# Optimization experiments

Hardware: AMD Instinct MI355X
Metric: run time of the kernel (lower is better)

Reference implementation:

```python
import jax, jax.numpy as jnp
import numpy as np


def setup_inputs() -> dict:
    key = jax.random.key(0)
    k1, k2, k3, k4 = jax.random.split(key, 4)
    B, C_in, C_out, E, K = 4, 128, 256, 30000, 5
    x = jax.random.normal(k1, (B, C_in, E, 1), dtype=jnp.float32)
    ne_idx = jax.random.randint(k2, (B, E, K - 1), 0, E, dtype=jnp.int32)
    conv_w = jax.random.normal(k3, (C_out, C_in, 1, K), dtype=jnp.float32) * 0.05
    conv_b = jax.random.normal(k4, (C_out,), dtype=jnp.float32) * 0.05
    return {"x": x, "ne_idx": ne_idx, "conv_w": conv_w, "conv_b": conv_b}


def reference(x, ne_idx, conv_w, conv_b):
    # x: [B, C, E, 1] edge features; ne_idx: [B, E, 4] neighbor edge ids.
    B, C, E, _ = x.shape
    xs = x[..., 0]                                        # [B, C, E]

    # pad_graph_mat: prepend self index column -> [B, E, 5]
    self_idx = jnp.broadcast_to(
        jnp.arange(E, dtype=ne_idx.dtype)[None, :, None], (B, E, 1))
    idx = jnp.concatenate([self_idx, ne_idx], axis=2) + 1  # +1 for zero pad slot

    # zero-pad feature dim so index 0 maps to zeros (matches torch padding col)
    x_pad = jnp.pad(xs, ((0, 0), (0, 0), (1, 0)))          # [B, C, E+1]

    # gather: f[b, c, e, k] = x_pad[b, c, idx[b, e, k]]
    f = jax.vmap(lambda xp, i: xp[:, i])(x_pad, idx)       # [B, C, E, 5]

    e0, e1, e2, e3, e4 = (f[..., j] for j in range(5))
    p = e1 + e3
    q = e2 + e4
    p1 = jnp.abs(e1 - e3)
    q1 = jnp.abs(e2 - e4)
    G = jnp.stack([e0, p, q, p1, q1], axis=-1)             # [B, C, E, 5]

    # Conv2d with kernel (1, 5): contraction over in-channels and the 5 taps
    out = jnp.einsum('bcek,ocuk->boe', G, conv_w) + conv_b[None, :, None]
    return out[..., None]                                  # [B, C_out, E, 1]
```

## Files before the change

kernel.cpp:

```cpp
#include <hip/hip_runtime.h>
#include <hip/hip_bf16.h>
#include <stdint.h>

#define E_N   30000
#define C_IN  128
#define C_OUT 256
#define B_N   4
#define KTAP  5
#define BN    64

typedef short bf16x8 __attribute__((ext_vector_type(8)));
typedef float f32x4  __attribute__((ext_vector_type(4)));

static __device__ __forceinline__ unsigned short f2bf(float f) {
    union { float f; uint32_t u; } v; v.f = f;
    uint32_t r = (v.u + 0x7FFFu + ((v.u >> 16) & 1u)) >> 16;
    return (unsigned short)r;
}
static __device__ __forceinline__ float bf2f(uint32_t h) {
    union { uint32_t u; float f; } v; v.u = h << 16;
    return v.f;
}

static __device__ __forceinline__ void comb8(const uint4& u, const uint4& v,
                                             uint4& s, uint4& d) {
    const uint32_t* a = (const uint32_t*)&u;
    const uint32_t* b = (const uint32_t*)&v;
    uint32_t* so = (uint32_t*)&s;
    uint32_t* dr = (uint32_t*)&d;
#pragma unroll
    for (int i = 0; i < 4; ++i) {
        float x0 = bf2f(a[i] & 0xFFFFu), x1 = bf2f(a[i] >> 16);
        float y0 = bf2f(b[i] & 0xFFFFu), y1 = bf2f(b[i] >> 16);
        so[i] = (uint32_t)f2bf(x0 + y0) | ((uint32_t)f2bf(x1 + y1) << 16);
        dr[i] = (uint32_t)f2bf(fabsf(x0 - y0)) | ((uint32_t)f2bf(fabsf(x1 - y1)) << 16);
    }
}

__global__ void pack_w_kernel(const float* __restrict__ w,
                              unsigned short* __restrict__ wp) {
    int tid = blockIdx.x * blockDim.x + threadIdx.x;
    if (tid >= 20 * 16 * 64) return;
    int s    = tid >> 10;
    int mt   = (tid >> 6) & 15;
    int lane = tid & 63;
    int m    = mt * 16 + (lane & 15);
    int kb   = s * 32 + ((lane >> 4) & 3) * 8;
    uint32_t pv[4];
    for (int jj = 0; jj < 4; ++jj) {
        unsigned short lo, hi;
        {
            int kk = kb + 2 * jj;
            int t = kk >> 7, c = kk & 127;
            lo = f2bf(w[(m * C_IN + c) * KTAP + t]);
        }
        {
            int kk = kb + 2 * jj + 1;
            int t = kk >> 7, c = kk & 127;
            hi = f2bf(w[(m * C_IN + c) * KTAP + t]);
        }
        pv[jj] = (uint32_t)lo | ((uint32_t)hi << 16);
    }
    uint4 val; val.x = pv[0]; val.y = pv[1]; val.z = pv[2]; val.w = pv[3];
    *(uint4*)(wp + (size_t)tid * 8) = val;
}

__global__ void transpose_kernel(const float* __restrict__ x,
                                 unsigned short* __restrict__ xT) {
    __shared__ float ld[C_IN][64 + 1];
    int b  = blockIdx.y;
    int e0 = blockIdx.x * 64;
    int t  = threadIdx.x;
    bool full = (e0 + 64 <= E_N);
    for (int pass = 0; pass < 8; ++pass) {
        int c  = pass * 16 + (t >> 4);
        int eo = (t & 15) * 4;
        if (full) {
            const float4 v = *(const float4*)(x + ((size_t)(b * C_IN + c) * E_N + e0 + eo));
            ld[c][eo] = v.x; ld[c][eo + 1] = v.y; ld[c][eo + 2] = v.z; ld[c][eo + 3] = v.w;
        } else {
            for (int i = 0; i < 4; ++i) {
                int e = e0 + eo + i;
                ld[c][eo + i] = (e < E_N) ? x[(size_t)(b * C_IN + c) * E_N + e] : 0.f;
            }
        }
    }
    __syncthreads();
    for (int pass = 0; pass < 4; ++pass) {
        int el = pass * 16 + (t >> 4);
        int c0 = (t & 15) * 8;
        int e  = e0 + el;
        if (e < E_N) {
            uint32_t pk[4];
            for (int i = 0; i < 4; ++i) {
                unsigned short lo = f2bf(ld[c0 + 2 * i][el]);
                unsigned short hi = f2bf(ld[c0 + 2 * i + 1][el]);
                pk[i] = (uint32_t)lo | ((uint32_t)hi << 16);
            }
            uint4 v; v.x = pk[0]; v.y = pk[1]; v.z = pk[2]; v.w = pk[3];
            *(uint4*)(xT + (size_t)(b * E_N + e) * C_IN + c0) = v;
        }
    }
}

__launch_bounds__(512, 4)
__global__ void mesh_gemm(const unsigned short* __restrict__ wp,
                          const unsigned short* __restrict__ xT,
                          const int* __restrict__ ne,
                          const float* __restrict__ bias,
                          float* __restrict__ out) {
    __shared__ uint4 gbuf[KTAP][BN][16];

    const int b    = blockIdx.y;
    const int e0   = blockIdx.x * BN;
    const int tid  = threadIdx.x;
    const int lane = tid & 63;
    const int wave = tid >> 6;

    {
        const int col = tid >> 3;
        const int ci  = tid & 7;
        int e = e0 + col; if (e >= E_N) e = E_N - 1;
        const int4 nb = *(const int4*)(ne + ((size_t)b * E_N + e) * 4);

        const unsigned short* xb = xT + (size_t)b * E_N * C_IN;
        const uint4* r0 = (const uint4*)(xb + (size_t)e    * C_IN) + ci;
        const uint4* r1 = (const uint4*)(xb + (size_t)nb.x * C_IN) + ci;
        const uint4* r2 = (const uint4*)(xb + (size_t)nb.y * C_IN) + ci;
        const uint4* r3 = (const uint4*)(xb + (size_t)nb.z * C_IN) + ci;
        const uint4* r4 = (const uint4*)(xb + (size_t)nb.w * C_IN) + ci;

        uint4 a0 = r0[0], a1 = r1[0], a2 = r2[0], a3 = r3[0], a4 = r4[0];
        uint4 b0 = r0[8], b1 = r1[8], b2 = r2[8], b3 = r3[8], b4 = r4[8];

        const int sw = col & 15;
        const int cl = ci ^ sw;
        const int ch = (ci + 8) ^ sw;

        uint4 s, d;
        gbuf[0][col][cl] = a0;
        comb8(a1, a3, s, d);  gbuf[1][col][cl] = s;  gbuf[3][col][cl] = d;
        comb8(a2, a4, s, d);  gbuf[2][col][cl] = s;  gbuf[4][col][cl] = d;
        gbuf[0][col][ch] = b0;
        comb8(b1, b3, s, d);  gbuf[1][col][ch] = s;  gbuf[3][col][ch] = d;
        comb8(b2, b4, s, d);  gbuf[2][col][ch] = s;  gbuf[4][col][ch] = d;
    }
    __syncthreads();

    f32x4 acc[2][4];
#pragma unroll
    for (int mt = 0; mt < 2; ++mt)
#pragma unroll
        for (int nt = 0; nt < 4; ++nt)
            acc[mt][nt] = (f32x4){0.f, 0.f, 0.f, 0.f};

    const uint4* wp16 = (const uint4*)wp;
    const int nl = lane & 15;
    const int kq = lane >> 4;

#pragma unroll 4
    for (int s = 0; s < 20; ++s) {
        const int tap = s >> 2, cbi = s & 3;
        uint4 w0 = wp16[(s * 16 + wave * 2 + 0) * 64 + lane];
        uint4 w1 = wp16[(s * 16 + wave * 2 + 1) * 64 + lane];
        bf16x8 af0 = *(bf16x8*)&w0;
        bf16x8 af1 = *(bf16x8*)&w1;
#pragma unroll
        for (int nt = 0; nt < 4; ++nt) {
            uint4 bv = gbuf[tap][nt * 16 + nl][((cbi << 2) + kq) ^ nl];
            bf16x8 bf = *(bf16x8*)&bv;
            acc[0][nt] = __builtin_amdgcn_mfma_f32_16x16x32_bf16(af0, bf, acc[0][nt], 0, 0, 0);
            acc[1][nt] = __builtin_amdgcn_mfma_f32_16x16x32_bf16(af1, bf, acc[1][nt], 0, 0, 0);
        }
    }

    const int quad = lane >> 4;
    const int ecol = lane & 15;
#pragma unroll
    for (int mt = 0; mt < 2; ++mt) {
        int ob = (wave * 2 + mt) * 16 + quad * 4;
#pragma unroll
        for (int r = 0; r < 4; ++r) {
            int o = ob + r;
            float bv = bias[o];
#pragma unroll
            for (int nt = 0; nt < 4; ++nt) {
                int e = e0 + nt * 16 + ecol;
                if (e < E_N)
                    out[((size_t)(b * C_OUT + o)) * E_N + e] = acc[mt][nt][r] + bv;
            }
        }
    }
}

__global__ void fallback_kernel(const float* __restrict__ x,
                                const int* __restrict__ ne,
                                const float* __restrict__ w,
                                const float* __restrict__ bias,
                                float* __restrict__ out) {
    size_t id = (size_t)blockIdx.x * blockDim.x + threadIdx.x;
    if (id >= (size_t)B_N * C_OUT * E_N) return;
    int e = (int)(id % E_N);
    int o = (int)((id / E_N) % C_OUT);
    int b = (int)(id / ((size_t)E_N * C_OUT));
    const int4 nb = *(const int4*)(ne + ((size_t)b * E_N + e) * 4);
    float acc = bias[o];
    for (int c = 0; c < C_IN; ++c) {
        const float* xb = x + (size_t)(b * C_IN + c) * E_N;
        float s0 = xb[e];
        float x1 = xb[nb.x], x2 = xb[nb.y], x3 = xb[nb.z], x4 = xb[nb.w];
        const float* wo = w + (size_t)(o * C_IN + c) * KTAP;
        acc += wo[0] * s0
             + wo[1] * (x1 + x3)
             + wo[2] * (x2 + x4)
             + wo[3] * fabsf(x1 - x3)
             + wo[4] * fabsf(x2 - x4);
    }
    out[id] = acc;
}

extern "C" void kernel_launch(void* const* d_in, const int* in_sizes, int n_in,
                              void* d_out, int out_size, void* d_ws, size_t ws_size,
                              hipStream_t stream) {
    const float* x      = (const float*)d_in[0];
    const int*   ne_idx = (const int*)d_in[1];
    const float* conv_w = (const float*)d_in[2];
    const float* conv_b = (const float*)d_in[3];
    float* out = (float*)d_out;

    const size_t xT_off = 512 * 1024;
    const size_t need   = xT_off + (size_t)B_N * E_N * C_IN * 2;

    if (ws_size < need) {
        size_t total = (size_t)B_N * C_OUT * E_N;
        int blocks = (int)((total + 255) / 256);
        fallback_kernel<<<blocks, 256, 0, stream>>>(x, ne_idx, conv_w, conv_b, out);
        return;
    }

    unsigned short* wp = (unsigned short*)d_ws;
    unsigned short* xT = (unsigned short*)((char*)d_ws + xT_off);

    pack_w_kernel<<<80, 256, 0, stream>>>(conv_w, wp);
    dim3 tg((E_N + 63) / 64, B_N);
    transpose_kernel<<<tg, 256, 0, stream>>>(x, xT);
    dim3 gg((E_N + BN - 1) / BN, B_N);
    mesh_gemm<<<gg, 512, 0, stream>>>(wp, xT, ne_idx, conv_b, out);
}
```

Before: 238.5 us.

## Process two batches per block, prefetching second gather during first MFMA pass

Each block now handles two batch indices instead of one, halving the grid's y-dimension. The gather loads for the second batch are issued into registers before the MFMA loop of the first batch runs, so global gather latency overlaps with compute. Bias values are loaded once per block and reused. In exchange the block count halves and each thread holds ten extra uint4 values in registers, which may reduce occupancy.

```diff
diff --git a/kernel.cpp b/kernel.cpp
--- a/kernel.cpp
+++ b/kernel.cpp
@@ -111,86 +111,107 @@
                           float* __restrict__ out) {
     __shared__ uint4 gbuf[KTAP][BN][16];
 
-    const int b    = blockIdx.y;
     const int e0   = blockIdx.x * BN;
     const int tid  = threadIdx.x;
     const int lane = tid & 63;
     const int wave = tid >> 6;
-
-    {
-        const int col = tid >> 3;
-        const int ci  = tid & 7;
-        int e = e0 + col; if (e >= E_N) e = E_N - 1;
-        const int4 nb = *(const int4*)(ne + ((size_t)b * E_N + e) * 4);
-
+    const int b0   = blockIdx.y * 2;
+    const int b1   = b0 + 1;
+
+    const int col = tid >> 3;
+    const int ci  = tid & 7;
+    int eg = e0 + col; if (eg >= E_N) eg = E_N - 1;
+
+    const int4 nb0 = *(const int4*)(ne + ((size_t)b0 * E_N + eg) * 4);
+    const int4 nb1 = *(const int4*)(ne + ((size_t)b1 * E_N + eg) * 4);
+
+    const int sw = col & 15;
+    const int cl = ci ^ sw;
+    const int ch = (ci + 8) ^ sw;
+
+    const uint4* wp16 = (const uint4*)wp;
+    const int nl   = lane & 15;
+    const int kq   = lane >> 4;
+    const int quad = kq;
+
+    float bvl[2][4];
+#pragma unroll
+    for (int mt = 0; mt < 2; ++mt)
+#pragma unroll
+        for (int r = 0; r < 4; ++r)
+            bvl[mt][r] = bias[(wave * 2 + mt) * 16 + quad * 4 + r];
+
+    auto gather10 = [&](int b, const int4& nb, uint4* g) {
         const unsigned short* xb = xT + (size_t)b * E_N * C_IN;
-        const uint4* r0 = (const uint4*)(xb + (size_t)e    * C_IN) + ci;
+        const uint4* r0 = (const uint4*)(xb + (size_t)eg   * C_IN) + ci;
         const uint4* r1 = (const uint4*)(xb + (size_t)nb.x * C_IN) + ci;
         const uint4* r2 = (const uint4*)(xb + (size_t)nb.y * C_IN) + ci;
         const uint4* r3 = (const uint4*)(xb + (size_t)nb.z * C_IN) + ci;
         const uint4* r4 = (const uint4*)(xb + (size_t)nb.w * C_IN) + ci;
-
-        uint4 a0 = r0[0], a1 = r1[0], a2 = r2[0], a3 = r3[0], a4 = r4[0];
-        uint4 b0 = r0[8], b1 = r1[8], b2 = r2[8], b3 = r3[8], b4 = r4[8];
-
-        const int sw = col & 15;
-        const int cl = ci ^ sw;
-        const int ch = (ci + 8) ^ sw;
-
+        g[0] = r0[0]; g[1] = r1[0]; g[2] = r2[0]; g[3] = r3[0]; g[4] = r4[0];
+        g[5] = r0[8]; g[6] = r1[8]; g[7] = r2[8]; g[8] = r3[8]; g[9] = r4[8];
+    };
+    auto combineStore = [&](uint4* g) {
         uint4 s, d;
-        gbuf[0][col][cl] = a0;
-        comb8(a1, a3, s, d);  gbuf[1][col][cl] = s;  gbuf[3][col][cl] = d;
-        comb8(a2, a4, s, d);  gbuf[2][col][cl] = s;  gbuf[4][col][cl] = d;
-        gbuf[0][col][ch] = b0;
-        comb8(b1, b3, s, d);  gbuf[1][col][ch] = s;  gbuf[3][col][ch] = d;
-        comb8(b2, b4, s, d);  gbuf[2][col][ch] = s;  gbuf[4][col][ch] = d;
-    }
-    __syncthreads();
-
-    f32x4 acc[2][4];
-#pragma unroll
-    for (int mt = 0; mt < 2; ++mt)
-#pragma unroll
-        for (int nt = 0; nt < 4; ++nt)
-            acc[mt][nt] = (f32x4){0.f, 0.f, 0.f, 0.f};
-
-    const uint4* wp16 = (const uint4*)wp;
-    const int nl = lane & 15;
-    const int kq = lane >> 4;
-
+        gbuf[0][col][cl] = g[0];
+        comb8(g[1], g[3], s, d); gbuf[1][col][cl] = s; gbuf[3][col][cl] = d;
+        comb8(g[2], g[4], s, d); gbuf[2][col][cl] = s; gbuf[4][col][cl] = d;
+        gbuf[0][col][ch] = g[5];
+        comb8(g[6], g[8], s, d); gbuf[1][col][ch] = s; gbuf[3][col][ch] = d;
+        comb8(g[7], g[9], s, d); gbuf[2][col][ch] = s; gbuf[4][col][ch] = d;
+    };
+    auto mfmaStore = [&](int b) {
+        f32x4 acc[2][4];
+#pragma unroll
+        for (int mt = 0; mt < 2; ++mt)
+#pragma unroll
+            for (int nt = 0; nt < 4; ++nt)
+                acc[mt][nt] = (f32x4){0.f, 0.f, 0.f, 0.f};
 #pragma unroll 4
-    for (int s = 0; s < 20; ++s) {
-        const int tap = s >> 2, cbi = s & 3;
-        uint4 w0 = wp16[(s * 16 + wave * 2 + 0) * 64 + lane];
-        uint4 w1 = wp16[(s * 16 + wave * 2 + 1) * 64 + lane];
-        bf16x8 af0 = *(bf16x8*)&w0;
-        bf16x8 af1 = *(bf16x8*)&w1;
-#pragma unroll
-        for (int nt = 0; nt < 4; ++nt) {
-            uint4 bv = gbuf[tap][nt * 16 + nl][((cbi << 2) + kq) ^ nl];
-            bf16x8 bf = *(bf16x8*)&bv;
-            acc[0][nt] = __builtin_amdgcn_mfma_f32_16x16x32_bf16(af0, bf, acc[0][nt], 0, 0, 0);
-            acc[1][nt] = __builtin_amdgcn_mfma_f32_16x16x32_bf16(af1, bf, acc[1][nt], 0, 0, 0);
-        }
-    }
-
-    const int quad = lane >> 4;
-    const int ecol = lane & 15;
-#pragma unroll
-    for (int mt = 0; mt < 2; ++mt) {
-        int ob = (wave * 2 + mt) * 16 + quad * 4;
-#pragma unroll
-        for (int r = 0; r < 4; ++r) {
-            int o = ob + r;
-            float bv = bias[o];
+        for (int s = 0; s < 20; ++s) {
+            const int tap = s >> 2, cbi = s & 3;
+            uint4 w0 = wp16[(s * 16 + wave * 2 + 0) * 64 + lane];
+            uint4 w1 = wp16[(s * 16 + wave * 2 + 1) * 64 + lane];
+            bf16x8 af0 = *(bf16x8*)&w0;
+            bf16x8 af1 = *(bf16x8*)&w1;
 #pragma unroll
             for (int nt = 0; nt < 4; ++nt) {
-                int e = e0 + nt * 16 + ecol;
-                if (e < E_N)
-                    out[((size_t)(b * C_OUT + o)) * E_N + e] = acc[mt][nt][r] + bv;
-            }
-        }
-    }
+                uint4 bv = gbuf[tap][nt * 16 + nl][((cbi << 2) + kq) ^ nl];
+                bf16x8 bf = *(bf16x8*)&bv;
+                acc[0][nt] = __builtin_amdgcn_mfma_f32_16x16x32_bf16(af0, bf, acc[0][nt], 0, 0, 0);
+                acc[1][nt] = __builtin_amdgcn_mfma_f32_16x16x32_bf16(af1, bf, acc[1][nt], 0, 0, 0);
+            }
+        }
+#pragma unroll
+        for (int mt = 0; mt < 2; ++mt) {
+            const int ob = (wave * 2 + mt) * 16 + quad * 4;
+#pragma unroll
+            for (int r = 0; r < 4; ++r) {
+                const int o = ob + r;
+                const float bv = bvl[mt][r];
+#pragma unroll
+                for (int nt = 0; nt < 4; ++nt) {
+                    const int e = e0 + nt * 16 + nl;
+                    if (e < E_N)
+                        out[((size_t)(b * C_OUT + o)) * E_N + e] = acc[mt][nt][r] + bv;
+                }
+            }
+        }
+    };
+
+    uint4 ga[10];
+    gather10(b0, nb0, ga);
+    combineStore(ga);
+    __syncthreads();
+
+    uint4 gb[10];
+    gather10(b1, nb1, gb);
+    mfmaStore(b0);
+
+    __syncthreads();
+    combineStore(gb);
+    __syncthreads();
+    mfmaStore(b1);
 }
 
 __global__ void fallback_kernel(const float* __restrict__ x,
@@ -244,6 +265,6 @@
     pack_w_kernel<<<80, 256, 0, stream>>>(conv_w, wp);
     dim3 tg((E_N + 63) / 64, B_N);
     transpose_kernel<<<tg, 256, 0, stream>>>(x, xT);
-    dim3 gg((E_N + BN - 1) / BN, B_N);
+    dim3 gg((E_N + BN - 1) / BN, B_N / 2);
     mesh_gemm<<<gg, 512, 0, stream>>>(wp, xT, ne_idx, conv_b, out);
 }
```

After: 225.8 us. -5.3%, faster.
